# Kernel tuning notes

Hardware: AMD Instinct MI355X
Metric: run time of the kernel (lower is better)

The kernel has to match this reference:

```python
import jax, jax.numpy as jnp
import numpy as np

TOL = 1e-14
K = 3            # patch_size (torch default)
PAD = (K - 1) // 2


def covsqrt_mean(feature, inverse=False):
    # feature: [b, c, h, w]; cov is the (unnormalized) Gram of zero-mean features.
    b, c = feature.shape[0], feature.shape[1]
    flat = feature.reshape(b, c, -1)
    mean = jnp.mean(flat, axis=2, keepdims=True)
    zm = flat - mean
    cov = jnp.einsum('bcn,bdn->bcd', zm, zm)                      # [b,c,c]
    evals, evecs = jnp.linalg.eigh(cov)                           # ascending, like torch.symeig
    p = -0.5 if inverse else 0.5
    mask = evals > TOL                                            # drop tiny eigenvalues (rank truncation)
    safe = jnp.where(mask, evals, 1.0)
    scaled = jnp.where(mask, safe ** p, 0.0)
    covsqrt = jnp.einsum('bij,bj,bkj->bik', evecs, scaled, evecs)
    return covsqrt, mean


def whitening(feature):
    b, c, h, w = feature.shape
    inv, mean = covsqrt_mean(feature, inverse=True)
    out = jnp.einsum('bij,bjn->bin', inv, feature.reshape(b, c, -1) - mean)
    return out.reshape(b, c, h, w)


def coloring(feature, target):
    b, c, h, w = feature.shape
    covsqrt, mean = covsqrt_mean(target, inverse=False)
    out = jnp.einsum('bij,bjn->bin', covsqrt, feature.reshape(b, c, -1)) + mean
    return out.reshape(b, c, h, w)


def extract_patches(feature, k, pad):
    # Mirrors F.pad + unfold(2,k,1).unfold(3,k,1): row-major (di, dj) patch order.
    b, c, h, w = feature.shape
    padded = jnp.pad(feature, ((0, 0), (0, 0), (pad, pad), (pad, pad)))
    patches = jnp.stack([padded[:, :, di:di + h, dj:dj + w]
                         for di in range(k) for dj in range(k)], axis=-1)
    return patches  # [b, c, h, w, k*k]


def deconv_norm(h, w, k, pad):
    # Overlap count of kxk patches at stride 1 == separable box convolution of ones.
    rc = np.convolve(np.ones(h, np.float32), np.ones(k, np.float32))
    cc = np.convolve(np.ones(w, np.float32), np.ones(k, np.float32))
    full = np.outer(rc, cc)
    if pad > 0:
        full = full[pad:-pad, pad:-pad]
    return jnp.asarray(full.reshape(1, 1, h, w))


def _forward(content_feature, style_feature, style_strength=1.0):
    nc = whitening(content_feature)
    ns = whitening(style_feature)
    b, c, h, w = nc.shape
    P = h * w  # number of style patches (stride 1, 'same' padding)

    # Style patches as dynamic conv kernels: [b, P, c, k*k]
    ker = extract_patches(ns, K, PAD).reshape(b, c, P, K * K).transpose(0, 2, 1, 3)
    knorm = jnp.sqrt(jnp.sum(ker * ker, axis=(2, 3), keepdims=True))  # [b,P,1,1]

    # Patch score = per-sample conv2d of content with normalized style kernels.
    cp = extract_patches(nc, K, PAD)                                  # [b,c,h,w,kk]
    score = jnp.einsum('bchwq,bpcq->bphw', cp, ker / knorm)           # [b,P,h,w]

    # Hard best-match per pixel (one-hot argmax in the original code).
    idx = jnp.argmax(score, axis=1).reshape(b, P)                     # [b, h*w]

    # Gather the matched UNnormalized style kernel for every pixel.
    ker5 = ker.reshape(b, P, c, K, K)
    sel = jnp.take_along_axis(ker5, idx[:, :, None, None, None], axis=1)
    sel = sel.reshape(b, h, w, c, K, K)

    # conv_transpose2d of the one-hot mask == scatter-add each matched patch
    # centered at its pixel; crop 'same' padding.
    full = jnp.zeros((b, c, h + K - 1, w + K - 1), dtype=nc.dtype)
    for di in range(K):
        for dj in range(K):
            full = full.at[:, :, di:di + h, dj:dj + w].add(
                jnp.transpose(sel[..., di, dj], (0, 3, 1, 2)))
    reassembled = full[:, :, PAD:PAD + h, PAD:PAD + w] / deconv_norm(h, w, K, PAD)

    stylized = coloring(reassembled, style_feature)
    return (1.0 - style_strength) * content_feature + style_strength * stylized


def setup_inputs() -> dict:
    key = jax.random.key(0)
    k1, k2 = jax.random.split(key)
    content_feature = jax.random.normal(k1, (4, 256, 64, 64), dtype=jnp.float32)
    style_feature = jax.random.normal(k2, (4, 256, 64, 64), dtype=jnp.float32)
    return {"content_feature": content_feature, "style_feature": style_feature}


def reference(content_feature, style_feature):
    return _forward(content_feature, style_feature)
```

## Files before the change

kernel.cpp:

```cpp
#include <hip/hip_runtime.h>
#include <stdint.h>

constexpr int NB = 4;
constexpr int NC = 256;
constexpr int HW = 64;
constexpr int NP = 4096;
constexpr int NM = 8;
constexpr int NS_ITERS = 7;
constexpr int NSLAB = 128;
constexpr int PSLAB = NP / NSLAB;
constexpr int KSPLIT = 8;
constexpr int KCHUNK = NP / KSPLIT;
constexpr int NTILE8 = 36;

constexpr float SPLIT_SCALE = 512.0f;
constexpr double COV_DESCALE = 1.0 / ((double)SPLIT_SCALE * (double)SPLIT_SCALE);

typedef __attribute__((ext_vector_type(8))) _Float16 h8v;
typedef __attribute__((ext_vector_type(4))) _Float16 h4v;
typedef __attribute__((ext_vector_type(4))) float f4v;

#define GLD16(lds, g)                                                        \
  __builtin_amdgcn_global_load_lds(                                          \
      (const __attribute__((address_space(1))) void*)(g),                    \
      (__attribute__((address_space(3))) void*)(lds), 16, 0, 0)

__device__ inline unsigned sortable_f32(float f) {
  unsigned u = __float_as_uint(f);
  return (u & 0x80000000u) ? ~u : (u | 0x80000000u);
}

__global__ __launch_bounds__(256) void meansplit_kernel(const float* __restrict__ content,
                                                        const float* __restrict__ style,
                                                        float* __restrict__ mean,
                                                        _Float16* __restrict__ Czh,
                                                        _Float16* __restrict__ Czl) {
  int id = blockIdx.x;
  int feat = id / (NB * NC);
  int bc = id % (NB * NC);
  const float* src = (feat ? style : content) + (size_t)bc * NP;
  int tid = threadIdx.x;
  float s = 0.f;
  for (int i = tid; i < NP; i += 256) s += src[i];
  __shared__ float red[256];
  red[tid] = s;
  __syncthreads();
  for (int st = 128; st > 0; st >>= 1) {
    if (tid < st) red[tid] += red[tid + st];
    __syncthreads();
  }
  float mu = red[0] * (1.0f / NP);
  if (tid == 0) mean[id] = mu;
  _Float16* oh = Czh + (size_t)id * NP;
  _Float16* ol = Czl + (size_t)id * NP;
  for (int f4 = tid; f4 < NP / 4; f4 += 256) {
    float4 v = *(const float4*)&src[f4 * 4];
    float vv[4] = {v.x, v.y, v.z, v.w};
    h4v h, l;
#pragma unroll
    for (int q = 0; q < 4; q++) {
      float sv = (vv[q] - mu) * SPLIT_SCALE;
      _Float16 hh = (_Float16)sv;
      h[q] = hh;
      l[q] = (_Float16)(sv - (float)hh);
    }
    *(h4v*)&oh[f4 * 4] = h;
    *(h4v*)&ol[f4 * 4] = l;
  }
}

__global__ __launch_bounds__(256) void cov_mfma_kernel(const _Float16* __restrict__ Czh,
                                                       const _Float16* __restrict__ Czl,
                                                       double* __restrict__ pcov) {
  __shared__ _Float16 sAh[64 * 32], sAl[64 * 32], sBh[64 * 32], sBl[64 * 32];
  int m = blockIdx.z;
  int t = blockIdx.x, ti = 0, rem = t;
  while (rem >= 4 - ti) { rem -= 4 - ti; ti++; }
  int tj = ti + rem;
  int i0 = ti * 64, j0 = tj * 64;
  const _Float16* Ah = Czh + ((size_t)m * NC + i0) * NP;
  const _Float16* Al = Czl + ((size_t)m * NC + i0) * NP;
  const _Float16* Bh = Czh + ((size_t)m * NC + j0) * NP;
  const _Float16* Bl = Czl + ((size_t)m * NC + j0) * NP;
  int k0base = blockIdx.y * KCHUNK;
  int tid = threadIdx.x, lane = tid & 63;
  int mm = lane & 15, quad = lane >> 4;
  int w = tid >> 6, qr = w & 1, qc = w >> 1;
  double dacc[2][2][4] = {};
  for (int step = 0; step < KCHUNK / 32; step++) {
    int k0 = k0base + step * 32;
    __syncthreads();
    {
      int row = tid >> 2, koff = (tid & 3) * 8;
      int sbase = (tid & ~63) * 8;
      GLD16(&sAh[sbase], Ah + (size_t)row * NP + k0 + koff);
      GLD16(&sAl[sbase], Al + (size_t)row * NP + k0 + koff);
      GLD16(&sBh[sbase], Bh + (size_t)row * NP + k0 + koff);
      GLD16(&sBl[sbase], Bl + (size_t)row * NP + k0 + koff);
    }
    __syncthreads();
    h8v afh[2], afl[2], bfh[2], bfl[2];
#pragma unroll
    for (int tt = 0; tt < 2; tt++) {
      int ra = (qr * 32 + tt * 16 + mm) * 32 + quad * 8;
      afh[tt] = *(const h8v*)&sAh[ra];
      afl[tt] = *(const h8v*)&sAl[ra];
      int rb = (qc * 32 + tt * 16 + mm) * 32 + quad * 8;
      bfh[tt] = *(const h8v*)&sBh[rb];
      bfl[tt] = *(const h8v*)&sBl[rb];
    }
    f4v acc[2][2] = {};
#pragma unroll
    for (int tr = 0; tr < 2; tr++)
#pragma unroll
      for (int tc = 0; tc < 2; tc++) {
        acc[tr][tc] = __builtin_amdgcn_mfma_f32_16x16x32_f16(afh[tr], bfh[tc], acc[tr][tc], 0, 0, 0);
        acc[tr][tc] = __builtin_amdgcn_mfma_f32_16x16x32_f16(afh[tr], bfl[tc], acc[tr][tc], 0, 0, 0);
        acc[tr][tc] = __builtin_amdgcn_mfma_f32_16x16x32_f16(afl[tr], bfh[tc], acc[tr][tc], 0, 0, 0);
        acc[tr][tc] = __builtin_amdgcn_mfma_f32_16x16x32_f16(afl[tr], bfl[tc], acc[tr][tc], 0, 0, 0);
      }
#pragma unroll
    for (int tr = 0; tr < 2; tr++)
#pragma unroll
      for (int tc = 0; tc < 2; tc++)
#pragma unroll
        for (int r = 0; r < 4; r++) dacc[tr][tc][r] += (double)acc[tr][tc][r];
  }
  double* dst = pcov + ((size_t)blockIdx.y * NM + m) * NC * NC;
#pragma unroll
  for (int tr = 0; tr < 2; tr++)
#pragma unroll
    for (int tc = 0; tc < 2; tc++)
#pragma unroll
      for (int r = 0; r < 4; r++) {
        int row = i0 + qr * 32 + tr * 16 + quad * 4 + r;
        int col = j0 + qc * 32 + tc * 16 + mm;
        dst[(size_t)row * NC + col] = dacc[tr][tc][r];
      }
}

__global__ __launch_bounds__(256) void cov_reduce_kernel(const double* __restrict__ pcov,
                                                         double* __restrict__ cov) {
  size_t idx = (size_t)blockIdx.x * 256 + threadIdx.x;
  int m = (int)(idx >> 16);
  int ij = (int)(idx & 65535);
  int i = ij >> 8, j = ij & 255;
  int src = ((i >> 6) <= (j >> 6)) ? ij : ((j << 8) | i);
  double s = 0;
  for (int k = 0; k < KSPLIT; k++)
    s += pcov[((size_t)k * NM + m) * 65536 + src];
  cov[idx] = s * COV_DESCALE;
}

__global__ __launch_bounds__(256) void bound_init_kernel(const double* __restrict__ cov,
                                                         float* __restrict__ Y,
                                                         float* __restrict__ Z,
                                                         double* __restrict__ scaleArr) {
  int m = blockIdx.x;
  const double* A = cov + (size_t)m * NC * NC;
  int t = threadIdx.x;
  double s = 0;
  for (int i = 0; i < NC; i++) s += fabs(A[(size_t)i * NC + t]);
  __shared__ double red[256];
  red[t] = s;
  __syncthreads();
  for (int st = 128; st > 0; st >>= 1) {
    if (t < st) red[t] = fmax(red[t], red[t + st]);
    __syncthreads();
  }
  double scale = 1.0 / red[0];
  if (t == 0) scaleArr[m] = scale;
  float* Ym = Y + (size_t)m * NC * NC;
  float* Zm = Z + (size_t)m * NC * NC;
  for (int idx = t; idx < NC * NC; idx += 256) {
    Ym[idx] = (float)(A[idx] * scale);
    Zm[idx] = ((idx / NC) == (idx % NC)) ? 1.0f : 0.0f;
  }
}


__global__ __launch_bounds__(256) void ns_t_kernel(const float* __restrict__ Zin,
                                                   const float* __restrict__ Yin,
                                                   float* __restrict__ T) {
  int m = blockIdx.z;
  const float* Am = Zin + (size_t)m * NC * NC;
  const float* Bm = Yin + (size_t)m * NC * NC;
  float* Tm = T + (size_t)m * NC * NC;
  __shared__ float As[32][33];
  __shared__ float Bs[32][33];
  int tid = threadIdx.x, tx = tid & 15, ty = tid >> 4;
  int t = blockIdx.x, ti = 0, rem = t;
  while (rem >= 8 - ti) { rem -= 8 - ti; ti++; }
  int tj = ti + rem;
  int i0 = ti * 32, j0 = tj * 32;
  float a00 = 0, a01 = 0, a10 = 0, a11 = 0;
  for (int k0 = 0; k0 < NC; k0 += 32) {
    for (int idx = tid; idx < 1024; idx += 256) {
      int r = idx >> 5, cc = idx & 31;
      As[r][cc] = Am[(size_t)(i0 + r) * NC + k0 + cc];
      Bs[r][cc] = Bm[(size_t)(k0 + r) * NC + j0 + cc];
    }
    __syncthreads();
#pragma unroll
    for (int kk = 0; kk < 32; kk++) {
      float x0 = As[ty * 2][kk], x1 = As[ty * 2 + 1][kk];
      float y0 = Bs[kk][tx * 2], y1 = Bs[kk][tx * 2 + 1];
      a00 += x0 * y0; a01 += x0 * y1; a10 += x1 * y0; a11 += x1 * y1;
    }
    __syncthreads();
  }
  Tm[(size_t)(i0 + ty * 2) * NC + j0 + tx * 2] = a00;
  Tm[(size_t)(i0 + ty * 2) * NC + j0 + tx * 2 + 1] = a01;
  Tm[(size_t)(i0 + ty * 2 + 1) * NC + j0 + tx * 2] = a10;
  Tm[(size_t)(i0 + ty * 2 + 1) * NC + j0 + tx * 2 + 1] = a11;
  if (ti != tj) {
    As[ty * 2][tx * 2] = a00;
    As[ty * 2][tx * 2 + 1] = a01;
    As[ty * 2 + 1][tx * 2] = a10;
    As[ty * 2 + 1][tx * 2 + 1] = a11;
    __syncthreads();
    for (int idx = tid; idx < 1024; idx += 256) {
      int r = idx >> 5, cc = idx & 31;
      Tm[(size_t)(j0 + r) * NC + i0 + cc] = As[cc][r];
    }
  }
}

__global__ __launch_bounds__(256) void ns_upd_kernel(const float* __restrict__ Yin,
                                                     const float* __restrict__ Zin,
                                                     const float* __restrict__ T,
                                                     float* __restrict__ Yout,
                                                     float* __restrict__ Zout) {
  int z = blockIdx.z;
  int m = z & 7, which = z >> 3;
  size_t off = (size_t)m * NC * NC;
  const float* Am = which == 0 ? (Yin + off) : (T + off);
  const float* Bm = which == 0 ? (T + off) : (Zin + off);
  const float* Sm = which == 0 ? (Yin + off) : (Zin + off);
  float* Om = which == 0 ? (Yout + off) : (Zout + off);
  __shared__ float As[32][33];
  __shared__ float Bs[32][33];
  int tid = threadIdx.x, tx = tid & 15, ty = tid >> 4;
  int t = blockIdx.x, ti = 0, rem = t;
  while (rem >= 8 - ti) { rem -= 8 - ti; ti++; }
  int tj = ti + rem;
  int i0 = ti * 32, j0 = tj * 32;
  float a00 = 0, a01 = 0, a10 = 0, a11 = 0;
  for (int k0 = 0; k0 < NC; k0 += 32) {
    for (int idx = tid; idx < 1024; idx += 256) {
      int r = idx >> 5, cc = idx & 31;
      As[r][cc] = Am[(size_t)(i0 + r) * NC + k0 + cc];
      Bs[r][cc] = Bm[(size_t)(k0 + r) * NC + j0 + cc];
    }
    __syncthreads();
#pragma unroll
    for (int kk = 0; kk < 32; kk++) {
      float x0 = As[ty * 2][kk], x1 = As[ty * 2 + 1][kk];
      float y0 = Bs[kk][tx * 2], y1 = Bs[kk][tx * 2 + 1];
      a00 += x0 * y0; a01 += x0 * y1; a10 += x1 * y0; a11 += x1 * y1;
    }
    __syncthreads();
  }
  int r0 = i0 + ty * 2, c0 = j0 + tx * 2;
  float o00 = 1.5f * Sm[(size_t)r0 * NC + c0] - 0.5f * a00;
  float o01 = 1.5f * Sm[(size_t)r0 * NC + c0 + 1] - 0.5f * a01;
  float o10 = 1.5f * Sm[(size_t)(r0 + 1) * NC + c0] - 0.5f * a10;
  float o11 = 1.5f * Sm[(size_t)(r0 + 1) * NC + c0 + 1] - 0.5f * a11;
  Om[(size_t)r0 * NC + c0] = o00;
  Om[(size_t)r0 * NC + c0 + 1] = o01;
  Om[(size_t)(r0 + 1) * NC + c0] = o10;
  Om[(size_t)(r0 + 1) * NC + c0 + 1] = o11;
  if (ti != tj) {
    As[ty * 2][tx * 2] = o00;
    As[ty * 2][tx * 2 + 1] = o01;
    As[ty * 2 + 1][tx * 2] = o10;
    As[ty * 2 + 1][tx * 2 + 1] = o11;
    __syncthreads();
    for (int idx = tid; idx < 1024; idx += 256) {
      int r = idx >> 5, cc = idx & 31;
      Om[(size_t)(j0 + r) * NC + i0 + cc] = As[cc][r];
    }
  }
}

__global__ __launch_bounds__(256) void finalize_kernel(const float* __restrict__ Yf,
                                                       const float* __restrict__ Zf,
                                                       const double* __restrict__ scaleArr,
                                                       float* __restrict__ inv_c,
                                                       float* __restrict__ inv_s,
                                                       float* __restrict__ sqr_s) {
  int which = blockIdx.y;
  int idx = blockIdx.x * 256 + threadIdx.x;
  int b = idx >> 16;
  int ij = idx & 65535;
  if (which == 0) {
    double s = sqrt(scaleArr[b]);
    inv_c[idx] = (float)((double)Zf[(size_t)b * 65536 + ij] * s);
  } else if (which == 1) {
    double s = sqrt(scaleArr[4 + b]);
    inv_s[idx] = (float)((double)Zf[(size_t)(4 + b) * 65536 + ij] * s);
  } else {
    double s = sqrt(scaleArr[4 + b]);
    sqr_s[idx] = (float)((double)Yf[(size_t)(4 + b) * 65536 + ij] / s);
  }
}

__global__ __launch_bounds__(256) void whiten_kernel(const float* __restrict__ content,
                                                     const float* __restrict__ style,
                                                     const float* __restrict__ mean,
                                                     const float* __restrict__ inv_c,
                                                     const float* __restrict__ inv_s,
                                                     float* __restrict__ ncwT,
                                                     float* __restrict__ nswT) {
  int z = blockIdx.z; int feat = z >> 2, b = z & 3;
  const float* src = (feat ? style : content) + (size_t)b * NC * NP;
  const float* mu = mean + (size_t)feat * NB * NC + b * NC;
  const float* M = (feat ? inv_s : inv_c) + (size_t)b * NC * NC;
  float* dst = (feat ? nswT : ncwT) + (size_t)b * NP * NC;
  int x0 = blockIdx.x * 128, c0 = blockIdx.y * 64;
  __shared__ float Ms[32][68];
  __shared__ float Xs[32][136];
  int tid = threadIdx.x, tx = tid & 15, ty = tid >> 4;
  float acc[8][4] = {};
  for (int k0 = 0; k0 < NC; k0 += 32) {
    for (int idx = tid; idx < 512; idx += 256) {
      int kk = idx >> 4, r4 = (idx & 15) * 4;
      *(float4*)&Ms[kk][r4] = *(const float4*)&M[(size_t)(k0 + kk) * NC + c0 + r4];
    }
    for (int idx = tid; idx < 1024; idx += 256) {
      int r = idx >> 5, c4 = (idx & 31) * 4;
      float4 v = *(const float4*)&src[(size_t)(k0 + r) * NP + x0 + c4];
      float mm = mu[k0 + r];
      v.x -= mm; v.y -= mm; v.z -= mm; v.w -= mm;
      *(float4*)&Xs[r][c4] = v;
    }
    __syncthreads();
#pragma unroll
    for (int kk = 0; kk < 32; kk++) {
      float4 xa = *(const float4*)&Xs[kk][ty * 8];
      float4 xb = *(const float4*)&Xs[kk][ty * 8 + 4];
      float4 mv = *(const float4*)&Ms[kk][tx * 4];
      float xv[8] = {xa.x, xa.y, xa.z, xa.w, xb.x, xb.y, xb.z, xb.w};
      float mm4[4] = {mv.x, mv.y, mv.z, mv.w};
#pragma unroll
      for (int i = 0; i < 8; i++)
#pragma unroll
        for (int j = 0; j < 4; j++) acc[i][j] += xv[i] * mm4[j];
    }
    __syncthreads();
  }
#pragma unroll
  for (int i = 0; i < 8; i++)
    *(float4*)&dst[(size_t)(x0 + ty * 8 + i) * NC + c0 + tx * 4] =
        make_float4(acc[i][0], acc[i][1], acc[i][2], acc[i][3]);
}

__global__ __launch_bounds__(256) void split_kernel(const float* __restrict__ ncwT,
                                                    const float* __restrict__ nswT,
                                                    _Float16* __restrict__ BhiT,
                                                    _Float16* __restrict__ BloT,
                                                    _Float16* __restrict__ AhiT,
                                                    _Float16* __restrict__ AloT,
                                                    float* __restrict__ ssq) {
  int z = blockIdx.z; int feat = z >> 2, b = z & 3;
  int wave = threadIdx.x >> 6, lane = threadIdx.x & 63;
  int y = blockIdx.x * 4 + wave;
  const float* src = (feat ? nswT : ncwT) + ((size_t)b * NP + y) * NC;
  _Float16* oh = (feat ? AhiT : BhiT) + ((size_t)b * NP + y) * NC;
  _Float16* ol = (feat ? AloT : BloT) + ((size_t)b * NP + y) * NC;
  float4 v = *(const float4*)&src[lane * 4];
  float vv[4] = {v.x, v.y, v.z, v.w};
  h4v h, l;
#pragma unroll
  for (int q = 0; q < 4; q++) {
    float sv = vv[q] * SPLIT_SCALE;
    _Float16 hh = (_Float16)sv;
    h[q] = hh;
    l[q] = (_Float16)(sv - (float)hh);
  }
  *(h4v*)&oh[lane * 4] = h;
  *(h4v*)&ol[lane * 4] = l;
  if (feat) {
    float s = vv[0] * vv[0] + vv[1] * vv[1] + vv[2] * vv[2] + vv[3] * vv[3];
#pragma unroll
    for (int off = 32; off > 0; off >>= 1) s += __shfl_down(s, off);
    if (lane == 0) ssq[b * NP + y] = s;
  }
}

__global__ __launch_bounds__(256) void rknorm_kernel(const float* __restrict__ ssq,
                                                     float* __restrict__ rk) {
  int idx = blockIdx.x * 256 + threadIdx.x;
  int b = idx >> 12, p = idx & 4095;
  int pi = p >> 6, pj = p & 63;
  float s = 0.f;
#pragma unroll
  for (int d = -1; d <= 1; d++)
#pragma unroll
    for (int e = -1; e <= 1; e++) {
      if ((unsigned)(pi + d) < 64u && (unsigned)(pj + e) < 64u)
        s += ssq[b * NP + (pi + d) * 64 + pj + e];
    }
  rk[idx] = 1.0f / sqrtf(s);
}

__global__ __launch_bounds__(256) void dmat_kernel(const _Float16* __restrict__ AhiT,
                                                   const _Float16* __restrict__ AloT,
                                                   const _Float16* __restrict__ BhiT,
                                                   const _Float16* __restrict__ BloT,
                                                   float* __restrict__ D, int b) {
  __shared__ _Float16 sAh[128 * 32], sAl[128 * 32], sBh[128 * 32], sBl[128 * 32];
  const _Float16* Ah = AhiT + (size_t)b * NP * NC;
  const _Float16* Al = AloT + (size_t)b * NP * NC;
  const _Float16* Bh = BhiT + (size_t)b * NP * NC;
  const _Float16* Bl = BloT + (size_t)b * NP * NC;
  int p0 = blockIdx.x * 128, x0 = blockIdx.y * 128;
  int tid = threadIdx.x, lane = tid & 63;
  int m = lane & 15, quad = lane >> 4;
  int w = tid >> 6, qr = w & 1, qc = w >> 1;
  f4v acc[4][4] = {};
  for (int step = 0; step < NC / 32; step++) {
    int c0 = step * 32;
    __syncthreads();
#pragma unroll
    for (int i = 0; i < 2; i++) {
      int seg = i * 256 + tid;
      int row = seg >> 2, koff = (seg & 3) * 8;
      int sbase = (i * 256 + (tid & ~63)) * 8;
      GLD16(&sAh[sbase], Ah + (size_t)(p0 + row) * NC + c0 + koff);
      GLD16(&sAl[sbase], Al + (size_t)(p0 + row) * NC + c0 + koff);
      GLD16(&sBh[sbase], Bh + (size_t)(x0 + row) * NC + c0 + koff);
      GLD16(&sBl[sbase], Bl + (size_t)(x0 + row) * NC + c0 + koff);
    }
    __syncthreads();
    h8v afh[4], afl[4], bfh[4], bfl[4];
#pragma unroll
    for (int t = 0; t < 4; t++) {
      int ra = (qr * 64 + t * 16 + m) * 32 + quad * 8;
      afh[t] = *(const h8v*)&sAh[ra];
      afl[t] = *(const h8v*)&sAl[ra];
      int rb = (qc * 64 + t * 16 + m) * 32 + quad * 8;
      bfh[t] = *(const h8v*)&sBh[rb];
      bfl[t] = *(const h8v*)&sBl[rb];
    }
#pragma unroll
    for (int tr = 0; tr < 4; tr++)
#pragma unroll
      for (int tc = 0; tc < 4; tc++) {
        acc[tr][tc] = __builtin_amdgcn_mfma_f32_16x16x32_f16(afh[tr], bfh[tc], acc[tr][tc], 0, 0, 0);
        acc[tr][tc] = __builtin_amdgcn_mfma_f32_16x16x32_f16(afh[tr], bfl[tc], acc[tr][tc], 0, 0, 0);
        acc[tr][tc] = __builtin_amdgcn_mfma_f32_16x16x32_f16(afl[tr], bfh[tc], acc[tr][tc], 0, 0, 0);
      }
  }
#pragma unroll
  for (int tr = 0; tr < 4; tr++)
#pragma unroll
    for (int tc = 0; tc < 4; tc++)
#pragma unroll
      for (int r = 0; r < 4; r++) {
        int row = p0 + qr * 64 + tr * 16 + quad * 4 + r;
        int col = x0 + qc * 64 + tc * 16 + m;
        D[(size_t)row * NP + col] = acc[tr][tc][r];
      }
}

__global__ __launch_bounds__(256) void score_kernel(const float* __restrict__ D,
                                                    const float* __restrict__ rk,
                                                    unsigned long long* __restrict__ packed,
                                                    int b) {
  int x = blockIdx.x * 256 + threadIdx.x;
  int slab = blockIdx.y;
  int xi = x >> 6, xj = x & 63;
  const float* rkb = rk + (size_t)b * NP;
  bool xm[9];
#pragma unroll
  for (int q = 0; q < 9; q++) {
    int d = q / 3 - 1, e = q % 3 - 1;
    xm[q] = ((unsigned)(xi + d) < 64u) && ((unsigned)(xj + e) < 64u);
  }
  float best = -1e30f;
  int bi = 0;
  int p0 = slab * PSLAB;
  for (int p = p0; p < p0 + PSLAB; p++) {
    int pi = p >> 6, pj = p & 63;
    float acc = 0.f;
#pragma unroll
    for (int q = 0; q < 9; q++) {
      int d = q / 3 - 1, e = q % 3 - 1;
      int off = d * 64 + e;
      bool ok = xm[q] && ((unsigned)(pi + d) < 64u) && ((unsigned)(pj + e) < 64u);
      int row = ok ? p + off : p;
      int col = ok ? x + off : x;
      float t = D[(size_t)row * NP + col];
      acc += ok ? t : 0.f;
    }
    float s = acc * rkb[p];
    if (s > best) { best = s; bi = p; }
  }
  unsigned long long key = ((unsigned long long)sortable_f32(best) << 32) |
                           (unsigned)(~(unsigned)bi);
  atomicMax(&packed[(size_t)b * NP + x], key);
}

__global__ __launch_bounds__(256) void reassemble_kernel(const float* __restrict__ nswT,
                                                         const unsigned long long* __restrict__ packed,
                                                         float* __restrict__ reass) {
  int by = blockIdx.x;
  int b = by >> 12, y = by & 4095;
  int yi = y >> 6, yj = y & 63;
  int t = threadIdx.x;
  float acc = 0.f;
#pragma unroll
  for (int oi = 0; oi < 3; oi++)
#pragma unroll
    for (int oj = 0; oj < 3; oj++) {
      int xi = yi + 1 - oi, xj = yj + 1 - oj;
      if ((unsigned)xi < 64u && (unsigned)xj < 64u) {
        unsigned long long v = packed[(size_t)b * NP + xi * 64 + xj];
        int p = (int)((~(unsigned)(v & 0xFFFFFFFFull)) & 4095u);
        int qi = (p >> 6) + oi - 1, qj = (p & 63) + oj - 1;
        if ((unsigned)qi < 64u && (unsigned)qj < 64u)
          acc += nswT[((size_t)b * NP + qi * 64 + qj) * NC + t];
      }
    }
  int cy = (yi == 0 || yi == 63) ? 2 : 3;
  int cx = (yj == 0 || yj == 63) ? 2 : 3;
  reass[((size_t)b * NP + y) * NC + t] = acc / (float)(cy * cx);
}

__global__ __launch_bounds__(256) void coloring_kernel(const float* __restrict__ sqr_s,
                                                       const float* __restrict__ reass,
                                                       const float* __restrict__ mean,
                                                       float* __restrict__ out) {
  int b = blockIdx.z;
  const float* A = sqr_s + (size_t)b * NC * NC;
  const float* Bm = reass + (size_t)b * NP * NC;
  const float* mu = mean + (size_t)NB * NC + b * NC;
  float* dst = out + (size_t)b * NC * NP;
  int c0 = blockIdx.x * 64, y0 = blockIdx.y * 64;
  __shared__ float As[32][68];
  __shared__ float Bs[32][66];
  int tid = threadIdx.x, tx = tid & 15, ty = tid >> 4;
  float acc[4][4] = {};
  for (int k0 = 0; k0 < NC; k0 += 32) {
    for (int idx = tid; idx < 512; idx += 256) {
      int kk = idx >> 4, r4 = (idx & 15) * 4;
      *(float4*)&As[kk][r4] = *(const float4*)&A[(size_t)(k0 + kk) * NC + c0 + r4];
    }
    for (int idx = tid; idx < 2048; idx += 256) {
      int r = idx >> 5, kk = idx & 31;
      Bs[kk][r] = Bm[(size_t)(y0 + r) * NC + k0 + kk];
    }
    __syncthreads();
#pragma unroll
    for (int kk = 0; kk < 32; kk++) {
      float4 av = *(const float4*)&As[kk][ty * 4];
      float a[4] = {av.x, av.y, av.z, av.w};
      float bb[4];
      *(float2*)&bb[0] = *(const float2*)&Bs[kk][tx * 4];
      *(float2*)&bb[2] = *(const float2*)&Bs[kk][tx * 4 + 2];
#pragma unroll
      for (int i = 0; i < 4; i++)
#pragma unroll
        for (int j = 0; j < 4; j++) acc[i][j] += a[i] * bb[j];
    }
    __syncthreads();
  }
#pragma unroll
  for (int i = 0; i < 4; i++) {
    float m = mu[c0 + ty * 4 + i];
    float4 v = make_float4(acc[i][0] + m, acc[i][1] + m, acc[i][2] + m, acc[i][3] + m);
    *(float4*)&dst[(size_t)(c0 + ty * 4 + i) * NP + y0 + tx * 4] = v;
  }
}

extern "C" void kernel_launch(void* const* d_in, const int* in_sizes, int n_in,
                              void* d_out, int out_size, void* d_ws, size_t ws_size,
                              hipStream_t stream) {
  (void)in_sizes; (void)n_in; (void)out_size; (void)ws_size;
  const float* content = (const float*)d_in[0];
  const float* style = (const float*)d_in[1];
  float* out = (float*)d_out;

  char* w = (char*)d_ws;
  auto alloc = [&](size_t bytes) -> void* {
    void* p = (void*)w;
    w += (bytes + 255) & ~(size_t)255;
    return p;
  };
  float* mean = (float*)alloc(2 * NB * NC * sizeof(float));
  double* pcov = (double*)alloc((size_t)KSPLIT * NM * NC * NC * sizeof(double));
  double* cov = (double*)alloc((size_t)NM * NC * NC * sizeof(double));
  float* Y0 = (float*)alloc((size_t)NM * NC * NC * sizeof(float));
  float* Z0 = (float*)alloc((size_t)NM * NC * NC * sizeof(float));
  float* Y1 = (float*)alloc((size_t)NM * NC * NC * sizeof(float));
  float* Z1 = (float*)alloc((size_t)NM * NC * NC * sizeof(float));
  float* T = (float*)alloc((size_t)NM * NC * NC * sizeof(float));
  double* scaleArr = (double*)alloc(NM * sizeof(double));
  float* inv_c = (float*)alloc((size_t)NB * NC * NC * sizeof(float));
  float* inv_s = (float*)alloc((size_t)NB * NC * NC * sizeof(float));
  float* sqr_s = (float*)alloc((size_t)NB * NC * NC * sizeof(float));
  float* ncwT = (float*)alloc((size_t)NB * NP * NC * sizeof(float));
  float* nswT = (float*)alloc((size_t)NB * NP * NC * sizeof(float));
  float* ssq = (float*)alloc((size_t)NB * NP * sizeof(float));
  float* rk = (float*)alloc((size_t)NB * NP * sizeof(float));
  unsigned long long* packed =
      (unsigned long long*)alloc((size_t)NB * NP * sizeof(unsigned long long));
  float* Dbuf = (float*)alloc((size_t)NP * NP * sizeof(float));
  float* reass = Dbuf + (size_t)NB * NP * NC;
  _Float16* Czh = (_Float16*)Dbuf;
  _Float16* Czl = Czh + (size_t)NM * NC * NP;
  _Float16* AhiT = (_Float16*)pcov;
  _Float16* AloT = AhiT + (size_t)NB * NP * NC;
  _Float16* BhiT = AloT + (size_t)NB * NP * NC;
  _Float16* BloT = BhiT + (size_t)NB * NP * NC;

  meansplit_kernel<<<2 * NB * NC, 256, 0, stream>>>(content, style, mean, Czh, Czl);
  cov_mfma_kernel<<<dim3(10, KSPLIT, NM), 256, 0, stream>>>(Czh, Czl, pcov);
  cov_reduce_kernel<<<NM * NC * NC / 256, 256, 0, stream>>>(pcov, cov);

  bound_init_kernel<<<NM, 256, 0, stream>>>(cov, Y0, Z0, scaleArr);
  float *Ya = Y0, *Za = Z0, *Yb = Y1, *Zb = Z1;
  for (int it = 0; it < NS_ITERS; it++) {
    ns_t_kernel<<<dim3(NTILE8, 1, NM), 256, 0, stream>>>(Za, Ya, T);
    ns_upd_kernel<<<dim3(NTILE8, 1, NM * 2), 256, 0, stream>>>(Ya, Za, T, Yb, Zb);
    float* tmp;
    tmp = Ya; Ya = Yb; Yb = tmp;
    tmp = Za; Za = Zb; Zb = tmp;
  }
  finalize_kernel<<<dim3(NB * NC * NC / 256, 3), 256, 0, stream>>>(Ya, Za, scaleArr,
                                                                   inv_c, inv_s, sqr_s);

  whiten_kernel<<<dim3(NP / 128, NC / 64, 2 * NB), 256, 0, stream>>>(
      content, style, mean, inv_c, inv_s, ncwT, nswT);

  split_kernel<<<dim3(NP / 4, 1, 2 * NB), 256, 0, stream>>>(ncwT, nswT,
                                                            BhiT, BloT, AhiT, AloT, ssq);
  rknorm_kernel<<<NB * NP / 256, 256, 0, stream>>>(ssq, rk);

  hipMemsetAsync(packed, 0, (size_t)NB * NP * sizeof(unsigned long long), stream);
  for (int b = 0; b < NB; b++) {
    dmat_kernel<<<dim3(NP / 128, NP / 128), 256, 0, stream>>>(AhiT, AloT, BhiT, BloT, Dbuf, b);
    score_kernel<<<dim3(NP / 256, NSLAB), 256, 0, stream>>>(Dbuf, rk, packed, b);
  }

  reassemble_kernel<<<NB * NP, 256, 0, stream>>>(nswT, packed, reass);

  coloring_kernel<<<dim3(NC / 64, NP / 64, NB), 256, 0, stream>>>(sqr_s, reass, mean, out);
}
```

Baseline: 962.8 us.

## Replace FP32 whitening GEMM with split-FP16 MFMA kernel fused with hi/lo split

```diff
diff --git a/kernel.cpp b/kernel.cpp
--- a/kernel.cpp
+++ b/kernel.cpp
@@ -150,6 +150,42 @@
   for (int k = 0; k < KSPLIT; k++)
     s += pcov[((size_t)k * NM + m) * 65536 + src];
   cov[idx] = s * COV_DESCALE;
+}
+
+__global__ __launch_bounds__(256) void transpose_kernel(const _Float16* __restrict__ Czh,
+                                                        const _Float16* __restrict__ Czl,
+                                                        _Float16* __restrict__ CzhT,
+                                                        _Float16* __restrict__ CzlT) {
+  __shared__ unsigned short th[64][72], tl[64][72];
+  int m = blockIdx.z;
+  int p0 = blockIdx.x * 64, k0 = blockIdx.y * 64;
+  int tid = threadIdx.x;
+  const unsigned short* src_h = (const unsigned short*)(Czh + (size_t)m * NC * NP);
+  const unsigned short* src_l = (const unsigned short*)(Czl + (size_t)m * NC * NP);
+#pragma unroll
+  for (int j = 0; j < 4; j++) {
+    int e = j * 1024 + tid * 4;
+    int kk = e >> 6, pp = e & 63;
+    ushort4 vh = *(const ushort4*)&src_h[(size_t)(k0 + kk) * NP + p0 + pp];
+    ushort4 vl = *(const ushort4*)&src_l[(size_t)(k0 + kk) * NP + p0 + pp];
+    *(ushort4*)&th[kk][pp] = vh;
+    *(ushort4*)&tl[kk][pp] = vl;
+  }
+  __syncthreads();
+  unsigned short* dst_h = (unsigned short*)(CzhT + (size_t)m * NP * NC);
+  unsigned short* dst_l = (unsigned short*)(CzlT + (size_t)m * NP * NC);
+#pragma unroll
+  for (int j = 0; j < 4; j++) {
+    int e = j * 1024 + tid * 4;
+    int pp = e >> 6, kk = e & 63;
+    ushort4 vh, vl;
+    vh.x = th[kk][pp];     vh.y = th[kk + 1][pp];
+    vh.z = th[kk + 2][pp]; vh.w = th[kk + 3][pp];
+    vl.x = tl[kk][pp];     vl.y = tl[kk + 1][pp];
+    vl.z = tl[kk + 2][pp]; vl.w = tl[kk + 3][pp];
+    *(ushort4*)&dst_h[(size_t)(p0 + pp) * NC + k0 + kk] = vh;
+    *(ushort4*)&dst_l[(size_t)(p0 + pp) * NC + k0 + kk] = vl;
+  }
 }
 
 __global__ __launch_bounds__(256) void bound_init_kernel(const double* __restrict__ cov,
@@ -286,109 +322,119 @@
 __global__ __launch_bounds__(256) void finalize_kernel(const float* __restrict__ Yf,
                                                        const float* __restrict__ Zf,
                                                        const double* __restrict__ scaleArr,
-                                                       float* __restrict__ inv_c,
-                                                       float* __restrict__ inv_s,
+                                                       _Float16* __restrict__ Mh,
+                                                       _Float16* __restrict__ Ml,
                                                        float* __restrict__ sqr_s) {
   int which = blockIdx.y;
   int idx = blockIdx.x * 256 + threadIdx.x;
-  int b = idx >> 16;
+  int m = idx >> 16;
   int ij = idx & 65535;
   if (which == 0) {
-    double s = sqrt(scaleArr[b]);
-    inv_c[idx] = (float)((double)Zf[(size_t)b * 65536 + ij] * s);
-  } else if (which == 1) {
-    double s = sqrt(scaleArr[4 + b]);
-    inv_s[idx] = (float)((double)Zf[(size_t)(4 + b) * 65536 + ij] * s);
+    double s = sqrt(scaleArr[m]);
+    float v = (float)((double)Zf[idx] * s) * SPLIT_SCALE;
+    _Float16 h = (_Float16)v;
+    Mh[idx] = h;
+    Ml[idx] = (_Float16)(v - (float)h);
   } else {
-    double s = sqrt(scaleArr[4 + b]);
-    sqr_s[idx] = (float)((double)Yf[(size_t)(4 + b) * 65536 + ij] / s);
-  }
-}
-
-__global__ __launch_bounds__(256) void whiten_kernel(const float* __restrict__ content,
-                                                     const float* __restrict__ style,
-                                                     const float* __restrict__ mean,
-                                                     const float* __restrict__ inv_c,
-                                                     const float* __restrict__ inv_s,
-                                                     float* __restrict__ ncwT,
-                                                     float* __restrict__ nswT) {
-  int z = blockIdx.z; int feat = z >> 2, b = z & 3;
-  const float* src = (feat ? style : content) + (size_t)b * NC * NP;
-  const float* mu = mean + (size_t)feat * NB * NC + b * NC;
-  const float* M = (feat ? inv_s : inv_c) + (size_t)b * NC * NC;
-  float* dst = (feat ? nswT : ncwT) + (size_t)b * NP * NC;
-  int x0 = blockIdx.x * 128, c0 = blockIdx.y * 64;
-  __shared__ float Ms[32][68];
-  __shared__ float Xs[32][136];
-  int tid = threadIdx.x, tx = tid & 15, ty = tid >> 4;
-  float acc[8][4] = {};
-  for (int k0 = 0; k0 < NC; k0 += 32) {
-    for (int idx = tid; idx < 512; idx += 256) {
-      int kk = idx >> 4, r4 = (idx & 15) * 4;
-      *(float4*)&Ms[kk][r4] = *(const float4*)&M[(size_t)(k0 + kk) * NC + c0 + r4];
-    }
-    for (int idx = tid; idx < 1024; idx += 256) {
-      int r = idx >> 5, c4 = (idx & 31) * 4;
-      float4 v = *(const float4*)&src[(size_t)(k0 + r) * NP + x0 + c4];
-      float mm = mu[k0 + r];
-      v.x -= mm; v.y -= mm; v.z -= mm; v.w -= mm;
-      *(float4*)&Xs[r][c4] = v;
-    }
-    __syncthreads();
-#pragma unroll
-    for (int kk = 0; kk < 32; kk++) {
-      float4 xa = *(const float4*)&Xs[kk][ty * 8];
-      float4 xb = *(const float4*)&Xs[kk][ty * 8 + 4];
-      float4 mv = *(const float4*)&Ms[kk][tx * 4];
-      float xv[8] = {xa.x, xa.y, xa.z, xa.w, xb.x, xb.y, xb.z, xb.w};
-      float mm4[4] = {mv.x, mv.y, mv.z, mv.w};
-#pragma unroll
-      for (int i = 0; i < 8; i++)
-#pragma unroll
-        for (int j = 0; j < 4; j++) acc[i][j] += xv[i] * mm4[j];
-    }
-    __syncthreads();
-  }
-#pragma unroll
-  for (int i = 0; i < 8; i++)
-    *(float4*)&dst[(size_t)(x0 + ty * 8 + i) * NC + c0 + tx * 4] =
-        make_float4(acc[i][0], acc[i][1], acc[i][2], acc[i][3]);
-}
-
-__global__ __launch_bounds__(256) void split_kernel(const float* __restrict__ ncwT,
-                                                    const float* __restrict__ nswT,
-                                                    _Float16* __restrict__ BhiT,
-                                                    _Float16* __restrict__ BloT,
-                                                    _Float16* __restrict__ AhiT,
-                                                    _Float16* __restrict__ AloT,
-                                                    float* __restrict__ ssq) {
-  int z = blockIdx.z; int feat = z >> 2, b = z & 3;
-  int wave = threadIdx.x >> 6, lane = threadIdx.x & 63;
-  int y = blockIdx.x * 4 + wave;
-  const float* src = (feat ? nswT : ncwT) + ((size_t)b * NP + y) * NC;
-  _Float16* oh = (feat ? AhiT : BhiT) + ((size_t)b * NP + y) * NC;
-  _Float16* ol = (feat ? AloT : BloT) + ((size_t)b * NP + y) * NC;
-  float4 v = *(const float4*)&src[lane * 4];
-  float vv[4] = {v.x, v.y, v.z, v.w};
-  h4v h, l;
-#pragma unroll
-  for (int q = 0; q < 4; q++) {
-    float sv = vv[q] * SPLIT_SCALE;
-    _Float16 hh = (_Float16)sv;
-    h[q] = hh;
-    l[q] = (_Float16)(sv - (float)hh);
-  }
-  *(h4v*)&oh[lane * 4] = h;
-  *(h4v*)&ol[lane * 4] = l;
-  if (feat) {
-    float s = vv[0] * vv[0] + vv[1] * vv[1] + vv[2] * vv[2] + vv[3] * vv[3];
-#pragma unroll
-    for (int off = 32; off > 0; off >>= 1) s += __shfl_down(s, off);
-    if (lane == 0) ssq[b * NP + y] = s;
-  }
-}
-
-__global__ __launch_bounds__(256) void rknorm_kernel(const float* __restrict__ ssq,
+    if (m >= NB) return;
+    double s = sqrt(scaleArr[4 + m]);
+    sqr_s[idx] = (float)((double)Yf[(size_t)(4 + m) * 65536 + ij] / s);
+  }
+}
+
+__global__ __launch_bounds__(256) void whiten_mfma_kernel(const _Float16* __restrict__ CzhT,
+                                                          const _Float16* __restrict__ CzlT,
+                                                          const _Float16* __restrict__ Mh,
+                                                          const _Float16* __restrict__ Ml,
+                                                          _Float16* __restrict__ BhiT,
+                                                          _Float16* __restrict__ BloT,
+                                                          _Float16* __restrict__ AhiT,
+                                                          _Float16* __restrict__ AloT,
+                                                          float* __restrict__ nswT,
+                                                          float* __restrict__ ssqp) {
+  __shared__ _Float16 sAh[128 * 32], sAl[128 * 32], sBh[128 * 32], sBl[128 * 32];
+  int m = blockIdx.z;
+  const _Float16* Ah = CzhT + (size_t)m * NP * NC;
+  const _Float16* Al = CzlT + (size_t)m * NP * NC;
+  const _Float16* Bh = Mh + (size_t)m * NC * NC;
+  const _Float16* Bl = Ml + (size_t)m * NC * NC;
+  int p0 = blockIdx.x * 128, c0 = blockIdx.y * 128;
+  int tid = threadIdx.x, lane = tid & 63;
+  int mm = lane & 15, quad = lane >> 4;
+  int w = tid >> 6, qr = w & 1, qc = w >> 1;
+  f4v acc[4][4] = {};
+  for (int step = 0; step < NC / 32; step++) {
+    int k0 = step * 32;
+    __syncthreads();
+#pragma unroll
+    for (int i = 0; i < 2; i++) {
+      int seg = i * 256 + tid;
+      int row = seg >> 2, koff = (seg & 3) * 8;
+      int sbase = (i * 256 + (tid & ~63)) * 8;
+      GLD16(&sAh[sbase], Ah + (size_t)(p0 + row) * NC + k0 + koff);
+      GLD16(&sAl[sbase], Al + (size_t)(p0 + row) * NC + k0 + koff);
+      GLD16(&sBh[sbase], Bh + (size_t)(c0 + row) * NC + k0 + koff);
+      GLD16(&sBl[sbase], Bl + (size_t)(c0 + row) * NC + k0 + koff);
+    }
+    __syncthreads();
+    h8v afh[4], afl[4], bfh[4], bfl[4];
+#pragma unroll
+    for (int t = 0; t < 4; t++) {
+      int ra = (qr * 64 + t * 16 + mm) * 32 + quad * 8;
+      afh[t] = *(const h8v*)&sAh[ra];
+      afl[t] = *(const h8v*)&sAl[ra];
+      int rb = (qc * 64 + t * 16 + mm) * 32 + quad * 8;
+      bfh[t] = *(const h8v*)&sBh[rb];
+      bfl[t] = *(const h8v*)&sBl[rb];
+    }
+#pragma unroll
+    for (int tr = 0; tr < 4; tr++)
+#pragma unroll
+      for (int tc = 0; tc < 4; tc++) {
+        acc[tr][tc] = __builtin_amdgcn_mfma_f32_16x16x32_f16(afh[tr], bfh[tc], acc[tr][tc], 0, 0, 0);
+        acc[tr][tc] = __builtin_amdgcn_mfma_f32_16x16x32_f16(afh[tr], bfl[tc], acc[tr][tc], 0, 0, 0);
+        acc[tr][tc] = __builtin_amdgcn_mfma_f32_16x16x32_f16(afl[tr], bfh[tc], acc[tr][tc], 0, 0, 0);
+      }
+  }
+  int feat = m >> 2, b = m & 3;
+  _Float16* oh = (feat ? AhiT : BhiT) + (size_t)b * NP * NC;
+  _Float16* ol = (feat ? AloT : BloT) + (size_t)b * NP * NC;
+  float* nsw = nswT + (size_t)b * NP * NC;
+  const float DSPL = 1.0f / SPLIT_SCALE;
+  const float DESC = DSPL * DSPL;
+#pragma unroll
+  for (int tr = 0; tr < 4; tr++)
+#pragma unroll
+    for (int r = 0; r < 4; r++) {
+      int p = p0 + qr * 64 + tr * 16 + quad * 4 + r;
+      float ps = 0.f;
+#pragma unroll
+      for (int tc = 0; tc < 4; tc++) {
+        int c = c0 + qc * 64 + tc * 16 + mm;
+        float a = acc[tr][tc][r];
+        float sv = a * DSPL;
+        _Float16 hh = (_Float16)sv;
+        size_t o = (size_t)p * NC + c;
+        oh[o] = hh;
+        ol[o] = (_Float16)(sv - (float)hh);
+        if (feat) {
+          float v = a * DESC;
+          nsw[o] = v;
+          ps += v * v;
+        }
+      }
+      if (feat) {
+        ps += __shfl_xor(ps, 1);
+        ps += __shfl_xor(ps, 2);
+        ps += __shfl_xor(ps, 4);
+        ps += __shfl_xor(ps, 8);
+        if (mm == 0)
+          ssqp[((size_t)(blockIdx.y * 2 + qc) * NB + b) * NP + p] = ps;
+      }
+    }
+}
+
+__global__ __launch_bounds__(256) void rknorm_kernel(const float* __restrict__ ssqp,
                                                      float* __restrict__ rk) {
   int idx = blockIdx.x * 256 + threadIdx.x;
   int b = idx >> 12, p = idx & 4095;
@@ -398,8 +444,11 @@
   for (int d = -1; d <= 1; d++)
 #pragma unroll
     for (int e = -1; e <= 1; e++) {
-      if ((unsigned)(pi + d) < 64u && (unsigned)(pj + e) < 64u)
-        s += ssq[b * NP + (pi + d) * 64 + pj + e];
+      if ((unsigned)(pi + d) < 64u && (unsigned)(pj + e) < 64u) {
+        int q = b * NP + (pi + d) * 64 + pj + e;
+#pragma unroll
+        for (int sl = 0; sl < 4; sl++) s += ssqp[(size_t)sl * NB * NP + q];
+      }
     }
   rk[idx] = 1.0f / sqrtf(s);
 }
@@ -597,12 +646,11 @@
   float* Z1 = (float*)alloc((size_t)NM * NC * NC * sizeof(float));
   float* T = (float*)alloc((size_t)NM * NC * NC * sizeof(float));
   double* scaleArr = (double*)alloc(NM * sizeof(double));
-  float* inv_c = (float*)alloc((size_t)NB * NC * NC * sizeof(float));
-  float* inv_s = (float*)alloc((size_t)NB * NC * NC * sizeof(float));
+  _Float16* Mh = (_Float16*)alloc((size_t)NM * NC * NC * sizeof(_Float16));
+  _Float16* Ml = (_Float16*)alloc((size_t)NM * NC * NC * sizeof(_Float16));
   float* sqr_s = (float*)alloc((size_t)NB * NC * NC * sizeof(float));
-  float* ncwT = (float*)alloc((size_t)NB * NP * NC * sizeof(float));
   float* nswT = (float*)alloc((size_t)NB * NP * NC * sizeof(float));
-  float* ssq = (float*)alloc((size_t)NB * NP * sizeof(float));
+  float* ssqp = (float*)alloc((size_t)4 * NB * NP * sizeof(float));
   float* rk = (float*)alloc((size_t)NB * NP * sizeof(float));
   unsigned long long* packed =
       (unsigned long long*)alloc((size_t)NB * NP * sizeof(unsigned long long));
@@ -610,6 +658,8 @@
   float* reass = Dbuf + (size_t)NB * NP * NC;
   _Float16* Czh = (_Float16*)Dbuf;
   _Float16* Czl = Czh + (size_t)NM * NC * NP;
+  _Float16* CzhT = Czh + (size_t)2 * NM * NC * NP;
+  _Float16* CzlT = CzhT + (size_t)NM * NC * NP;
   _Float16* AhiT = (_Float16*)pcov;
   _Float16* AloT = AhiT + (size_t)NB * NP * NC;
   _Float16* BhiT = AloT + (size_t)NB * NP * NC;
@@ -618,6 +668,8 @@
   meansplit_kernel<<<2 * NB * NC, 256, 0, stream>>>(content, style, mean, Czh, Czl);
   cov_mfma_kernel<<<dim3(10, KSPLIT, NM), 256, 0, stream>>>(Czh, Czl, pcov);
   cov_reduce_kernel<<<NM * NC * NC / 256, 256, 0, stream>>>(pcov, cov);
+
+  transpose_kernel<<<dim3(NP / 64, NC / 64, NM), 256, 0, stream>>>(Czh, Czl, CzhT, CzlT);
 
   bound_init_kernel<<<NM, 256, 0, stream>>>(cov, Y0, Z0, scaleArr);
   float *Ya = Y0, *Za = Z0, *Yb = Y1, *Zb = Z1;
@@ -628,15 +680,13 @@
     tmp = Ya; Ya = Yb; Yb = tmp;
     tmp = Za; Za = Zb; Zb = tmp;
   }
-  finalize_kernel<<<dim3(NB * NC * NC / 256, 3), 256, 0, stream>>>(Ya, Za, scaleArr,
-                                                                   inv_c, inv_s, sqr_s);
-
-  whiten_kernel<<<dim3(NP / 128, NC / 64, 2 * NB), 256, 0, stream>>>(
-      content, style, mean, inv_c, inv_s, ncwT, nswT);
-
-  split_kernel<<<dim3(NP / 4, 1, 2 * NB), 256, 0, stream>>>(ncwT, nswT,
-                                                            BhiT, BloT, AhiT, AloT, ssq);
-  rknorm_kernel<<<NB * NP / 256, 256, 0, stream>>>(ssq, rk);
+  finalize_kernel<<<dim3(NM * NC * NC / 256, 2), 256, 0, stream>>>(Ya, Za, scaleArr,
+                                                                   Mh, Ml, sqr_s);
+
+  whiten_mfma_kernel<<<dim3(NP / 128, NC / 128, NM), 256, 0, stream>>>(
+      CzhT, CzlT, Mh, Ml, BhiT, BloT, AhiT, AloT, nswT, ssqp);
+
+  rknorm_kernel<<<NB * NP / 256, 256, 0, stream>>>(ssqp, rk);
 
   hipMemsetAsync(packed, 0, (size_t)NB * NP * sizeof(unsigned long long), stream);
   for (int b = 0; b < NB; b++) {
```

Measured after the change: 906.2 us. 5.9% less time.
